# Performance work log

Measured on AMD Instinct MI355X. Metric: run time of the kernel, lower is better.

The kernel has to match this reference:

```python
import jax, jax.numpy as jnp
import numpy as np

N = 50000      # nodes
E = 1600000    # edges (avg degree 32)
R = 8          # relation types
G = 64         # graphs in batch
D_IN = 128
HID = 128
CLS = 10


def setup_inputs() -> dict:
    key = jax.random.key(0)
    ks = jax.random.split(key, 12)
    s = 0.05  # weight init scale
    return {
        "x": jax.random.normal(ks[0], (N, D_IN), dtype=jnp.float32),
        "edge_index": jax.random.randint(ks[1], (2, E), 0, N, dtype=jnp.int32),
        "edge_type": jax.random.randint(ks[2], (E,), 0, R, dtype=jnp.int32),
        "batch": jnp.sort(jax.random.randint(ks[3], (N,), 0, G, dtype=jnp.int32)),
        "W1": jax.random.normal(ks[4], (R, D_IN, HID), dtype=jnp.float32) * s,
        "root1": jax.random.normal(ks[5], (D_IN, HID), dtype=jnp.float32) * s,
        "b1": jax.random.normal(ks[6], (HID,), dtype=jnp.float32) * s,
        "W2": jax.random.normal(ks[7], (R, HID, HID), dtype=jnp.float32) * s,
        "root2": jax.random.normal(ks[8], (HID, HID), dtype=jnp.float32) * s,
        "b2": jax.random.normal(ks[9], (HID,), dtype=jnp.float32) * s,
        "lin_w": jax.random.normal(ks[10], (HID, CLS), dtype=jnp.float32) * s,
        "lin_b": jax.random.normal(ks[11], (CLS,), dtype=jnp.float32) * s,
    }


def rgcn_conv(x, edge_index, edge_type, W, root, bias):
    # PyG RGCNConv (default aggr='mean'): per-relation mean of neighbor
    # features, relation-specific matmul, summed over relations, + root + bias.
    src, dst = edge_index[0], edge_index[1]
    d_in = x.shape[1]
    seg = dst * R + edge_type                      # fused (node, relation) segment id
    msg = jax.ops.segment_sum(x[src], seg, num_segments=N * R)          # [N*R, d_in]
    cnt = jax.ops.segment_sum(jnp.ones((E,), x.dtype), seg, num_segments=N * R)
    mean = (msg / jnp.maximum(cnt, 1.0)[:, None]).reshape(N, R, d_in)   # [N, R, d_in]
    return jnp.einsum('nrd,rdh->nh', mean, W) + x @ root + bias


def reference(x, edge_index, edge_type, batch, W1, root1, b1, W2, root2, b2, lin_w, lin_b):
    h = jax.nn.relu(rgcn_conv(x, edge_index, edge_type, W1, root1, b1))
    h = jax.nn.relu(rgcn_conv(h, edge_index, edge_type, W2, root2, b2))
    # global mean pool per graph
    gsum = jax.ops.segment_sum(h, batch, num_segments=G)                # [G, HID]
    gcnt = jax.ops.segment_sum(jnp.ones((N,), h.dtype), batch, num_segments=G)
    g = gsum / jnp.maximum(gcnt, 1.0)[:, None]
    return g @ lin_w + lin_b                                            # [G, CLS]
```

## Files before the change

kernel.cpp:

```cpp
#include <hip/hip_runtime.h>

#define N_NODES 50000
#define N_EDGES 1600000
#define R_REL 8
#define G_GRAPHS 64
#define D_INF 128
#define HIDF 128
#define CLSF 10

#define S_SEG (N_NODES * R_REL)
#define RZ 9
#define PCHUNK 16

#define XG 8
#define NODES_PER_G (N_NODES / XG)
#define SORT_BLKS_PER_G 256
#define SORT_GRID (XG * SORT_BLKS_PER_G)

typedef __attribute__((ext_vector_type(8))) short short8;
typedef __attribute__((ext_vector_type(4))) float floatx4;

typedef __attribute__((address_space(1))) const unsigned int guint;
typedef __attribute__((address_space(3))) unsigned int luint;
__device__ __forceinline__ void gload_lds16(const void* g, void* l) {
    __builtin_amdgcn_global_load_lds((guint*)g, (luint*)l, 16, 0, 0);
}

__device__ __forceinline__ unsigned short f2bf(float f) {
    unsigned int u = __float_as_uint(f);
    unsigned int r = (u + 0x7fffu + ((u >> 16) & 1u)) >> 16;
    return (unsigned short)r;
}
__device__ __forceinline__ float bflo(unsigned int u) { return __uint_as_float(u << 16); }
__device__ __forceinline__ float bfhi(unsigned int u) { return __uint_as_float(u & 0xffff0000u); }

__global__ __launch_bounds__(256) void count_kernel(const int* __restrict__ dst,
                                                    const int* __restrict__ et,
                                                    int* __restrict__ cnt) {
    int xg = blockIdx.x & (XG - 1);
    int inner = blockIdx.x >> 3;
    int lo = xg * NODES_PER_G, hi = lo + NODES_PER_G;
    for (int e = inner * 256 + threadIdx.x; e < N_EDGES; e += SORT_BLKS_PER_G * 256) {
        int d = dst[e];
        if (d >= lo && d < hi) {
            atomicAdd(&cnt[d * R_REL + et[e]], 1);
        }
    }
}

#define SCAN_BLK 256
#define SCAN_ELEMS 1024
#define NB_SCAN ((S_SEG + SCAN_ELEMS - 1) / SCAN_ELEMS)

__global__ __launch_bounds__(SCAN_BLK) void scan1_kernel(const int* __restrict__ cnt,
                                                         int* __restrict__ off,
                                                         int* __restrict__ bsum) {
    __shared__ int sd[SCAN_BLK];
    int t = threadIdx.x;
    int base = blockIdx.x * SCAN_ELEMS + t * 4;
    int v[4];
    int tsum = 0;
#pragma unroll
    for (int j = 0; j < 4; j++) {
        v[j] = (base + j < S_SEG) ? cnt[base + j] : 0;
        tsum += v[j];
    }
    sd[t] = tsum;
    __syncthreads();
    for (int d = 1; d < SCAN_BLK; d <<= 1) {
        int x = (t >= d) ? sd[t - d] : 0;
        __syncthreads();
        sd[t] += x;
        __syncthreads();
    }
    int incl = sd[t];
    int run = incl - tsum;
#pragma unroll
    for (int j = 0; j < 4; j++) {
        if (base + j < S_SEG) off[base + j] = run;
        run += v[j];
    }
    if (t == SCAN_BLK - 1) bsum[blockIdx.x] = incl;
}

__global__ __launch_bounds__(512) void scan2_kernel(int* __restrict__ bsum) {
    __shared__ int sd[512];
    int t = threadIdx.x;
    int v = (t < NB_SCAN) ? bsum[t] : 0;
    sd[t] = v;
    __syncthreads();
    for (int d = 1; d < 512; d <<= 1) {
        int x = (t >= d) ? sd[t - d] : 0;
        __syncthreads();
        sd[t] += x;
        __syncthreads();
    }
    if (t < NB_SCAN) bsum[t] = sd[t] - v;
}

__global__ void absoff_kernel(int* __restrict__ off, const int* __restrict__ bsum,
                              const int* __restrict__ cnt, float* __restrict__ winv) {
    int i = blockIdx.x * blockDim.x + threadIdx.x;
    if (i < S_SEG) {
        off[i] += bsum[i >> 10];
        winv[i] = 1.0f / (float)max(cnt[i], 1);
    }
}

__global__ __launch_bounds__(256) void bin_kernel(const int* __restrict__ src,
                                                  const int* __restrict__ dst,
                                                  const int* __restrict__ et,
                                                  const float* __restrict__ winv,
                                                  int* __restrict__ cursor,
                                                  int2* __restrict__ zw) {
    int xg = blockIdx.x & (XG - 1);
    int inner = blockIdx.x >> 3;
    int lo = xg * NODES_PER_G, hi = lo + NODES_PER_G;
    for (int e = inner * 256 + threadIdx.x; e < N_EDGES; e += SORT_BLKS_PER_G * 256) {
        int d = dst[e];
        if (d >= lo && d < hi) {
            int t = et[e];
            int seg = d * R_REL + t;
            int pos = atomicAdd(&cursor[seg], 1);
            zw[pos] = make_int2((src[e] * RZ + t) << 7, __float_as_int(winv[seg]));
        }
    }
}

__global__ void convx_kernel(const float* __restrict__ x, unsigned short* __restrict__ xb) {
    int idx = blockIdx.x * blockDim.x + threadIdx.x;
    if (idx < N_NODES * D_INF) xb[idx] = f2bf(x[idx]);
}

__global__ __launch_bounds__(256) void convw9_kernel(const float* __restrict__ W,
                                                     const float* __restrict__ root,
                                                     unsigned short* __restrict__ wz) {
    __shared__ float t[16][17];
    int r = blockIdx.z;
    int k0 = blockIdx.x * 16, c0 = blockIdx.y * 16;
    int tx = threadIdx.x & 15, ty = threadIdx.x >> 4;
    const float* srcp = (r < 8) ? (W + (size_t)r * 128 * 128) : root;
    t[ty][tx] = srcp[(size_t)(k0 + ty) * 128 + c0 + tx];
    __syncthreads();
    wz[(size_t)r * 16384 + (size_t)(c0 + ty) * 128 + k0 + tx] = f2bf(t[tx][ty]);
}

__global__ __launch_bounds__(256) void transform_gemm(
    const unsigned short* __restrict__ hb,
    const unsigned short* __restrict__ wz,
    unsigned short* __restrict__ z)
{
    __shared__ __align__(16) unsigned short A4[4][128][32];
    __shared__ __align__(16) unsigned short Bc[128][32];

    const int tx = threadIdx.x;
    const int wave = tx >> 6, lane = tx & 63;
    const int quad = lane >> 4, lq = lane & 15;
    const int row0 = blockIdx.x * 128;
    const int srow = lane >> 2;
    const int sch  = lane & 3;

#pragma unroll
    for (int kk = 0; kk < 4; kk++) {
#pragma unroll
        for (int p = 0; p < 2; p++) {
            int rr = (wave * 2 + p) * 16;
            int gr = row0 + rr + srow; if (gr >= N_NODES) gr = N_NODES - 1;
            gload_lds16(hb + (size_t)gr * HIDF + kk * 32 + sch * 8, &A4[kk][rr][0]);
        }
    }

    floatx4 acc[2][8];
    for (int r = 0; r < RZ; r++) {
#pragma unroll
        for (int i = 0; i < 2; i++)
#pragma unroll
            for (int j = 0; j < 8; j++) acc[i][j] = (floatx4){0.f, 0.f, 0.f, 0.f};

#pragma unroll
        for (int kk = 0; kk < 4; kk++) {
#pragma unroll
            for (int p = 0; p < 2; p++) {
                int cc = (wave * 2 + p) * 16;
                int gc = cc + srow;
                gload_lds16(wz + ((size_t)r * 128 + gc) * 128 + kk * 32 + sch * 8,
                            &Bc[cc][0]);
            }
            __syncthreads();

            short8 af[2], bfr[8];
#pragma unroll
            for (int i = 0; i < 2; i++)
                af[i] = *(const short8*)(&A4[kk][wave * 32 + i * 16 + lq][quad * 8]);
#pragma unroll
            for (int j = 0; j < 8; j++)
                bfr[j] = *(const short8*)(&Bc[j * 16 + lq][quad * 8]);
#pragma unroll
            for (int i = 0; i < 2; i++)
#pragma unroll
                for (int j = 0; j < 8; j++)
                    acc[i][j] = __builtin_amdgcn_mfma_f32_16x16x32_bf16(af[i], bfr[j], acc[i][j], 0, 0, 0);
            __syncthreads();
        }

#pragma unroll
        for (int i = 0; i < 2; i++) {
#pragma unroll
            for (int j = 0; j < 8; j++) {
                int col = j * 16 + lq;
#pragma unroll
                for (int rg = 0; rg < 4; rg++) {
                    int row = row0 + wave * 32 + i * 16 + quad * 4 + rg;
                    if (row < N_NODES)
                        z[((size_t)row * RZ + r) * 128 + col] = f2bf(acc[i][j][rg]);
                }
            }
        }
    }
}

__global__ __launch_bounds__(256) void agg2_kernel(const unsigned short* __restrict__ z,
                                                   const int2* __restrict__ zw,
                                                   const int* __restrict__ off,
                                                   const float* __restrict__ bias,
                                                   unsigned short* __restrict__ hout) {
    int nod = blockIdx.x * 8 + (threadIdx.x >> 5);
    if (nod >= N_NODES) return;
    int c = threadIdx.x & 31;
    int beg = off[nod * R_REL];
    int end = (nod < N_NODES - 1) ? off[(nod + 1) * R_REL] : N_EDGES;

    float a0 = 0.f, a1 = 0.f, a2 = 0.f, a3 = 0.f;
    int e = beg;
    for (; e + 4 <= end; e += 4) {
        int2 r0 = zw[e + 0], r1 = zw[e + 1], r2 = zw[e + 2], r3 = zw[e + 3];
        float w0 = __int_as_float(r0.y), w1 = __int_as_float(r1.y);
        float w2 = __int_as_float(r2.y), w3 = __int_as_float(r3.y);
        uint2 v0 = *(const uint2*)(z + (size_t)r0.x + c * 4);
        uint2 v1 = *(const uint2*)(z + (size_t)r1.x + c * 4);
        uint2 v2 = *(const uint2*)(z + (size_t)r2.x + c * 4);
        uint2 v3 = *(const uint2*)(z + (size_t)r3.x + c * 4);
        a0 += bflo(v0.x) * w0 + bflo(v1.x) * w1 + bflo(v2.x) * w2 + bflo(v3.x) * w3;
        a1 += bfhi(v0.x) * w0 + bfhi(v1.x) * w1 + bfhi(v2.x) * w2 + bfhi(v3.x) * w3;
        a2 += bflo(v0.y) * w0 + bflo(v1.y) * w1 + bflo(v2.y) * w2 + bflo(v3.y) * w3;
        a3 += bfhi(v0.y) * w0 + bfhi(v1.y) * w1 + bfhi(v2.y) * w2 + bfhi(v3.y) * w3;
    }
    for (; e < end; e++) {
        int2 rr = zw[e];
        float w = __int_as_float(rr.y);
        uint2 v = *(const uint2*)(z + (size_t)rr.x + c * 4);
        a0 += bflo(v.x) * w; a1 += bfhi(v.x) * w;
        a2 += bflo(v.y) * w; a3 += bfhi(v.y) * w;
    }
    uint2 vr = *(const uint2*)(z + ((size_t)nod * RZ + 8) * 128 + c * 4);
    a0 += bflo(vr.x); a1 += bfhi(vr.x); a2 += bflo(vr.y); a3 += bfhi(vr.y);
    float4 b = *(const float4*)(bias + c * 4);
    a0 = fmaxf(a0 + b.x, 0.0f);
    a1 = fmaxf(a1 + b.y, 0.0f);
    a2 = fmaxf(a2 + b.z, 0.0f);
    a3 = fmaxf(a3 + b.w, 0.0f);
    uint2 o;
    o.x = (unsigned int)f2bf(a0) | ((unsigned int)f2bf(a1) << 16);
    o.y = (unsigned int)f2bf(a2) | ((unsigned int)f2bf(a3) << 16);
    *(uint2*)(hout + (size_t)nod * HIDF + c * 4) = o;
}

__global__ __launch_bounds__(256) void pool1_kernel(const unsigned short* __restrict__ h,
                                                    const int* __restrict__ batch,
                                                    float* __restrict__ partial) {
    int g = blockIdx.x;
    int p = blockIdx.y;
    int lo, hi;
    {
        int l = 0, r = N_NODES;
        while (l < r) { int m = (l + r) >> 1; if (batch[m] < g) l = m + 1; else r = m; }
        lo = l;
        l = lo; r = N_NODES;
        while (l < r) { int m = (l + r) >> 1; if (batch[m] < g + 1) l = m + 1; else r = m; }
        hi = l;
    }
    int t = threadIdx.x;
    int rowlane = t >> 5;
    int c4 = t & 31;
    float a0 = 0.f, a1 = 0.f, a2 = 0.f, a3 = 0.f;
    for (int n = lo + p + rowlane * PCHUNK; n < hi; n += 8 * PCHUNK) {
        uint2 v = *(const uint2*)(h + (size_t)n * HIDF + c4 * 4);
        a0 += bflo(v.x); a1 += bfhi(v.x); a2 += bflo(v.y); a3 += bfhi(v.y);
    }
    __shared__ float red[8][128];
    if (rowlane == 0) {
        red[0][c4 * 4 + 0] = a0; red[0][c4 * 4 + 1] = a1;
        red[0][c4 * 4 + 2] = a2; red[0][c4 * 4 + 3] = a3;
    }
    __syncthreads();
    for (int s = 1; s < 8; s++) {
        if (rowlane == s) {
            red[0][c4 * 4 + 0] += a0; red[0][c4 * 4 + 1] += a1;
            red[0][c4 * 4 + 2] += a2; red[0][c4 * 4 + 3] += a3;
        }
        __syncthreads();
    }
    if (t < 128) partial[((size_t)g * PCHUNK + p) * 128 + t] = red[0][t];
}

__global__ __launch_bounds__(128) void pool2_kernel(const float* __restrict__ partial,
                                                    const int* __restrict__ batch,
                                                    float* __restrict__ gmean) {
    int g = blockIdx.x;
    int lo, hi;
    {
        int l = 0, r = N_NODES;
        while (l < r) { int m = (l + r) >> 1; if (batch[m] < g) l = m + 1; else r = m; }
        lo = l;
        l = lo; r = N_NODES;
        while (l < r) { int m = (l + r) >> 1; if (batch[m] < g + 1) l = m + 1; else r = m; }
        hi = l;
    }
    int t = threadIdx.x;
    float s = 0.f;
#pragma unroll
    for (int p = 0; p < PCHUNK; p++)
        s += partial[((size_t)g * PCHUNK + p) * 128 + t];
    gmean[g * HIDF + t] = s / (float)max(hi - lo, 1);
}

__global__ void final_kernel(const float* __restrict__ gmean,
                             const float* __restrict__ lin_w,
                             const float* __restrict__ lin_b,
                             float* __restrict__ out) {
    __shared__ float gl[HIDF];
    int g = blockIdx.x;
    int hh = threadIdx.x;
    gl[hh] = gmean[g * HIDF + hh];
    __syncthreads();
    if (hh < CLSF) {
        float s = lin_b[hh];
#pragma unroll 16
        for (int d = 0; d < HIDF; d++) s += gl[d] * lin_w[d * CLSF + hh];
        out[g * CLSF + hh] = s;
    }
}

extern "C" void kernel_launch(void* const* d_in, const int* in_sizes, int n_in,
                              void* d_out, int out_size, void* d_ws, size_t ws_size,
                              hipStream_t stream) {
    const float* x     = (const float*)d_in[0];
    const int*   ei    = (const int*)d_in[1];
    const int*   et    = (const int*)d_in[2];
    const int*   batch = (const int*)d_in[3];
    const float* W1    = (const float*)d_in[4];
    const float* root1 = (const float*)d_in[5];
    const float* b1    = (const float*)d_in[6];
    const float* W2    = (const float*)d_in[7];
    const float* root2 = (const float*)d_in[8];
    const float* b2    = (const float*)d_in[9];
    const float* lin_w = (const float*)d_in[10];
    const float* lin_b = (const float*)d_in[11];
    float* out = (float*)d_out;

    const int* src = ei;
    const int* dst = ei + N_EDGES;

    char* ws = (char*)d_ws;
    unsigned short* xb  = (unsigned short*)ws; ws += (size_t)N_NODES * HIDF * 2;
    unsigned short* h1  = (unsigned short*)ws; ws += (size_t)N_NODES * HIDF * 2;
    unsigned short* h2  = (unsigned short*)ws; ws += (size_t)N_NODES * HIDF * 2;
    unsigned short* z   = (unsigned short*)ws; ws += (size_t)N_NODES * RZ * 128 * 2;
    unsigned short* wz1 = (unsigned short*)ws; ws += (size_t)RZ * 128 * 128 * 2;
    unsigned short* wz2 = (unsigned short*)ws; ws += (size_t)RZ * 128 * 128 * 2;
    int*   cnt    = (int*)ws;   ws += (size_t)S_SEG * 4;
    int*   off    = (int*)ws;   ws += (size_t)S_SEG * 4;
    int*   bsum   = (int*)ws;   ws += 512 * 4;
    int*   cursor = (int*)ws;   ws += (size_t)S_SEG * 4;
    float* winv   = (float*)ws; ws += (size_t)S_SEG * 4;
    int2*  zw     = (int2*)ws;  ws += (size_t)N_EDGES * 8;
    float* partial = (float*)ws; ws += (size_t)G_GRAPHS * PCHUNK * 128 * 4;
    float* gmean  = (float*)ws; ws += (size_t)G_GRAPHS * HIDF * 4;

    hipMemsetAsync(cnt, 0, (size_t)S_SEG * 4, stream);

    count_kernel<<<SORT_GRID, 256, 0, stream>>>(dst, et, cnt);
    scan1_kernel<<<NB_SCAN, SCAN_BLK, 0, stream>>>(cnt, off, bsum);
    scan2_kernel<<<1, 512, 0, stream>>>(bsum);
    absoff_kernel<<<(S_SEG + 255) / 256, 256, 0, stream>>>(off, bsum, cnt, winv);
    hipMemcpyAsync(cursor, off, (size_t)S_SEG * 4, hipMemcpyDeviceToDevice, stream);
    bin_kernel<<<SORT_GRID, 256, 0, stream>>>(src, dst, et, winv, cursor, zw);

    convx_kernel<<<(N_NODES * D_INF + 255) / 256, 256, 0, stream>>>(x, xb);
    convw9_kernel<<<dim3(8, 8, RZ), 256, 0, stream>>>(W1, root1, wz1);
    convw9_kernel<<<dim3(8, 8, RZ), 256, 0, stream>>>(W2, root2, wz2);

    const int NGB = (N_NODES + 127) / 128;
    const int NAB = (N_NODES + 7) / 8;

    transform_gemm<<<NGB, 256, 0, stream>>>(xb, wz1, z);
    agg2_kernel<<<NAB, 256, 0, stream>>>(z, zw, off, b1, h1);

    transform_gemm<<<NGB, 256, 0, stream>>>(h1, wz2, z);
    agg2_kernel<<<NAB, 256, 0, stream>>>(z, zw, off, b2, h2);

    pool1_kernel<<<dim3(G_GRAPHS, PCHUNK), 256, 0, stream>>>(h2, batch, partial);
    pool2_kernel<<<G_GRAPHS, 128, 0, stream>>>(partial, batch, gmean);
    final_kernel<<<G_GRAPHS, HIDF, 0, stream>>>(gmean, lin_w, lin_b, out);

    (void)in_sizes; (void)n_in; (void)out_size; (void)ws_size;
}
```

Measured before the change: 488.7 us.

## Pack edge records into 4-byte indices, fuse cursor copy, retile transform GEMM

Each edge record shrinks from an int2 (z offset plus weight) to one int that packs the z offset with the relation type in its low bits. The aggregation kernel now looks up the per-(node, relation) inverse count from a small shared-memory table, which halves edge-list traffic in both aggregation passes. The cursor initialisation moves from a separate device-to-device memcpy into absoff_kernel. The transform GEMM switches to 64-row tiles and loads all four K-slices of B per relation before a single barrier, which doubles the grid and cuts syncs but reuses each loaded B tile across fewer rows.

```diff
diff --git a/kernel.cpp b/kernel.cpp
--- a/kernel.cpp
+++ b/kernel.cpp
@@ -99,10 +99,13 @@
 }
 
 __global__ void absoff_kernel(int* __restrict__ off, const int* __restrict__ bsum,
-                              const int* __restrict__ cnt, float* __restrict__ winv) {
+                              const int* __restrict__ cnt, float* __restrict__ winv,
+                              int* __restrict__ cursor) {
     int i = blockIdx.x * blockDim.x + threadIdx.x;
     if (i < S_SEG) {
-        off[i] += bsum[i >> 10];
+        int v = off[i] + bsum[i >> 10];
+        off[i] = v;
+        cursor[i] = v;
         winv[i] = 1.0f / (float)max(cnt[i], 1);
     }
 }
@@ -110,9 +113,8 @@
 __global__ __launch_bounds__(256) void bin_kernel(const int* __restrict__ src,
                                                   const int* __restrict__ dst,
                                                   const int* __restrict__ et,
-                                                  const float* __restrict__ winv,
                                                   int* __restrict__ cursor,
-                                                  int2* __restrict__ zw) {
+                                                  int* __restrict__ zidx) {
     int xg = blockIdx.x & (XG - 1);
     int inner = blockIdx.x >> 3;
     int lo = xg * NODES_PER_G, hi = lo + NODES_PER_G;
@@ -122,7 +124,7 @@
             int t = et[e];
             int seg = d * R_REL + t;
             int pos = atomicAdd(&cursor[seg], 1);
-            zw[pos] = make_int2((src[e] * RZ + t) << 7, __float_as_int(winv[seg]));
+            zidx[pos] = ((src[e] * RZ + t) << 7) | t;
         }
     }
 }
@@ -150,105 +152,101 @@
     const unsigned short* __restrict__ wz,
     unsigned short* __restrict__ z)
 {
-    __shared__ __align__(16) unsigned short A4[4][128][32];
-    __shared__ __align__(16) unsigned short Bc[128][32];
+    __shared__ __align__(16) unsigned short A4[4][64][32];
+    __shared__ __align__(16) unsigned short B4[4][128][32];
 
     const int tx = threadIdx.x;
     const int wave = tx >> 6, lane = tx & 63;
     const int quad = lane >> 4, lq = lane & 15;
-    const int row0 = blockIdx.x * 128;
+    const int row0 = blockIdx.x * 64;
     const int srow = lane >> 2;
     const int sch  = lane & 3;
 
 #pragma unroll
     for (int kk = 0; kk < 4; kk++) {
-#pragma unroll
-        for (int p = 0; p < 2; p++) {
-            int rr = (wave * 2 + p) * 16;
-            int gr = row0 + rr + srow; if (gr >= N_NODES) gr = N_NODES - 1;
-            gload_lds16(hb + (size_t)gr * HIDF + kk * 32 + sch * 8, &A4[kk][rr][0]);
-        }
-    }
-
-    floatx4 acc[2][8];
+        int gr = row0 + wave * 16 + srow; if (gr >= N_NODES) gr = N_NODES - 1;
+        gload_lds16(hb + (size_t)gr * HIDF + kk * 32 + sch * 8, &A4[kk][wave * 16][0]);
+    }
+
+    floatx4 acc[8];
     for (int r = 0; r < RZ; r++) {
-#pragma unroll
-        for (int i = 0; i < 2; i++)
-#pragma unroll
-            for (int j = 0; j < 8; j++) acc[i][j] = (floatx4){0.f, 0.f, 0.f, 0.f};
-
 #pragma unroll
         for (int kk = 0; kk < 4; kk++) {
 #pragma unroll
             for (int p = 0; p < 2; p++) {
                 int cc = (wave * 2 + p) * 16;
-                int gc = cc + srow;
-                gload_lds16(wz + ((size_t)r * 128 + gc) * 128 + kk * 32 + sch * 8,
-                            &Bc[cc][0]);
+                gload_lds16(wz + ((size_t)r * 128 + cc + srow) * 128 + kk * 32 + sch * 8,
+                            &B4[kk][cc][0]);
             }
-            __syncthreads();
-
-            short8 af[2], bfr[8];
-#pragma unroll
-            for (int i = 0; i < 2; i++)
-                af[i] = *(const short8*)(&A4[kk][wave * 32 + i * 16 + lq][quad * 8]);
-#pragma unroll
-            for (int j = 0; j < 8; j++)
-                bfr[j] = *(const short8*)(&Bc[j * 16 + lq][quad * 8]);
-#pragma unroll
-            for (int i = 0; i < 2; i++)
-#pragma unroll
-                for (int j = 0; j < 8; j++)
-                    acc[i][j] = __builtin_amdgcn_mfma_f32_16x16x32_bf16(af[i], bfr[j], acc[i][j], 0, 0, 0);
-            __syncthreads();
-        }
-
-#pragma unroll
-        for (int i = 0; i < 2; i++) {
+        }
+        __syncthreads();
+
+#pragma unroll
+        for (int j = 0; j < 8; j++) acc[j] = (floatx4){0.f, 0.f, 0.f, 0.f};
+#pragma unroll
+        for (int kk = 0; kk < 4; kk++) {
+            short8 af = *(const short8*)(&A4[kk][wave * 16 + lq][quad * 8]);
 #pragma unroll
             for (int j = 0; j < 8; j++) {
-                int col = j * 16 + lq;
-#pragma unroll
-                for (int rg = 0; rg < 4; rg++) {
-                    int row = row0 + wave * 32 + i * 16 + quad * 4 + rg;
-                    if (row < N_NODES)
-                        z[((size_t)row * RZ + r) * 128 + col] = f2bf(acc[i][j][rg]);
-                }
+                short8 bfr = *(const short8*)(&B4[kk][j * 16 + lq][quad * 8]);
+                acc[j] = __builtin_amdgcn_mfma_f32_16x16x32_bf16(af, bfr, acc[j], 0, 0, 0);
             }
         }
+
+#pragma unroll
+        for (int j = 0; j < 8; j++) {
+            int col = j * 16 + lq;
+#pragma unroll
+            for (int rg = 0; rg < 4; rg++) {
+                int row = row0 + wave * 16 + quad * 4 + rg;
+                if (row < N_NODES)
+                    z[((size_t)row * RZ + r) * 128 + col] = f2bf(acc[j][rg]);
+            }
+        }
+        __syncthreads();
     }
 }
 
 __global__ __launch_bounds__(256) void agg2_kernel(const unsigned short* __restrict__ z,
-                                                   const int2* __restrict__ zw,
+                                                   const int* __restrict__ zidx,
+                                                   const float* __restrict__ winv,
                                                    const int* __restrict__ off,
                                                    const float* __restrict__ bias,
                                                    unsigned short* __restrict__ hout) {
-    int nod = blockIdx.x * 8 + (threadIdx.x >> 5);
+    __shared__ float swinv[64];
+    int nod0 = blockIdx.x * 8;
+    if (threadIdx.x < 64) {
+        int idx = nod0 * R_REL + threadIdx.x;
+        swinv[threadIdx.x] = (idx < S_SEG) ? winv[idx] : 1.0f;
+    }
+    __syncthreads();
+
+    int hw = threadIdx.x >> 5;
+    int nod = nod0 + hw;
     if (nod >= N_NODES) return;
     int c = threadIdx.x & 31;
     int beg = off[nod * R_REL];
     int end = (nod < N_NODES - 1) ? off[(nod + 1) * R_REL] : N_EDGES;
+    const float* wl = &swinv[hw * 8];
 
     float a0 = 0.f, a1 = 0.f, a2 = 0.f, a3 = 0.f;
     int e = beg;
     for (; e + 4 <= end; e += 4) {
-        int2 r0 = zw[e + 0], r1 = zw[e + 1], r2 = zw[e + 2], r3 = zw[e + 3];
-        float w0 = __int_as_float(r0.y), w1 = __int_as_float(r1.y);
-        float w2 = __int_as_float(r2.y), w3 = __int_as_float(r3.y);
-        uint2 v0 = *(const uint2*)(z + (size_t)r0.x + c * 4);
-        uint2 v1 = *(const uint2*)(z + (size_t)r1.x + c * 4);
-        uint2 v2 = *(const uint2*)(z + (size_t)r2.x + c * 4);
-        uint2 v3 = *(const uint2*)(z + (size_t)r3.x + c * 4);
+        int p0 = zidx[e + 0], p1 = zidx[e + 1], p2 = zidx[e + 2], p3 = zidx[e + 3];
+        float w0 = wl[p0 & 7], w1 = wl[p1 & 7], w2 = wl[p2 & 7], w3 = wl[p3 & 7];
+        uint2 v0 = *(const uint2*)(z + (size_t)(p0 & 0x7FFFFF80) + c * 4);
+        uint2 v1 = *(const uint2*)(z + (size_t)(p1 & 0x7FFFFF80) + c * 4);
+        uint2 v2 = *(const uint2*)(z + (size_t)(p2 & 0x7FFFFF80) + c * 4);
+        uint2 v3 = *(const uint2*)(z + (size_t)(p3 & 0x7FFFFF80) + c * 4);
         a0 += bflo(v0.x) * w0 + bflo(v1.x) * w1 + bflo(v2.x) * w2 + bflo(v3.x) * w3;
         a1 += bfhi(v0.x) * w0 + bfhi(v1.x) * w1 + bfhi(v2.x) * w2 + bfhi(v3.x) * w3;
         a2 += bflo(v0.y) * w0 + bflo(v1.y) * w1 + bflo(v2.y) * w2 + bflo(v3.y) * w3;
         a3 += bfhi(v0.y) * w0 + bfhi(v1.y) * w1 + bfhi(v2.y) * w2 + bfhi(v3.y) * w3;
     }
     for (; e < end; e++) {
-        int2 rr = zw[e];
-        float w = __int_as_float(rr.y);
-        uint2 v = *(const uint2*)(z + (size_t)rr.x + c * 4);
+        int p = zidx[e];
+        float w = wl[p & 7];
+        uint2 v = *(const uint2*)(z + (size_t)(p & 0x7FFFFF80) + c * 4);
         a0 += bflo(v.x) * w; a1 += bfhi(v.x) * w;
         a2 += bflo(v.y) * w; a3 += bfhi(v.y) * w;
     }
@@ -373,7 +371,7 @@
     int*   bsum   = (int*)ws;   ws += 512 * 4;
     int*   cursor = (int*)ws;   ws += (size_t)S_SEG * 4;
     float* winv   = (float*)ws; ws += (size_t)S_SEG * 4;
-    int2*  zw     = (int2*)ws;  ws += (size_t)N_EDGES * 8;
+    int*   zidx   = (int*)ws;   ws += (size_t)N_EDGES * 4;
     float* partial = (float*)ws; ws += (size_t)G_GRAPHS * PCHUNK * 128 * 4;
     float* gmean  = (float*)ws; ws += (size_t)G_GRAPHS * HIDF * 4;
 
@@ -382,22 +380,21 @@
     count_kernel<<<SORT_GRID, 256, 0, stream>>>(dst, et, cnt);
     scan1_kernel<<<NB_SCAN, SCAN_BLK, 0, stream>>>(cnt, off, bsum);
     scan2_kernel<<<1, 512, 0, stream>>>(bsum);
-    absoff_kernel<<<(S_SEG + 255) / 256, 256, 0, stream>>>(off, bsum, cnt, winv);
-    hipMemcpyAsync(cursor, off, (size_t)S_SEG * 4, hipMemcpyDeviceToDevice, stream);
-    bin_kernel<<<SORT_GRID, 256, 0, stream>>>(src, dst, et, winv, cursor, zw);
+    absoff_kernel<<<(S_SEG + 255) / 256, 256, 0, stream>>>(off, bsum, cnt, winv, cursor);
+    bin_kernel<<<SORT_GRID, 256, 0, stream>>>(src, dst, et, cursor, zidx);
 
     convx_kernel<<<(N_NODES * D_INF + 255) / 256, 256, 0, stream>>>(x, xb);
     convw9_kernel<<<dim3(8, 8, RZ), 256, 0, stream>>>(W1, root1, wz1);
     convw9_kernel<<<dim3(8, 8, RZ), 256, 0, stream>>>(W2, root2, wz2);
 
-    const int NGB = (N_NODES + 127) / 128;
+    const int NGB = (N_NODES + 63) / 64;
     const int NAB = (N_NODES + 7) / 8;
 
     transform_gemm<<<NGB, 256, 0, stream>>>(xb, wz1, z);
-    agg2_kernel<<<NAB, 256, 0, stream>>>(z, zw, off, b1, h1);
+    agg2_kernel<<<NAB, 256, 0, stream>>>(z, zidx, winv, off, b1, h1);
 
     transform_gemm<<<NGB, 256, 0, stream>>>(h1, wz2, z);
-    agg2_kernel<<<NAB, 256, 0, stream>>>(z, zw, off, b2, h2);
+    agg2_kernel<<<NAB, 256, 0, stream>>>(z, zidx, winv, off, b2, h2);
 
     pool1_kernel<<<dim3(G_GRAPHS, PCHUNK), 256, 0, stream>>>(h2, batch, partial);
     pool2_kernel<<<G_GRAPHS, 128, 0, stream>>>(partial, batch, gmean);
```

After: 498.0 us. Within noise of the previous version (+1.9%).
